# Kernel optimization log

Hardware: AMD Instinct MI355X
Metric: run time of the kernel (lower is better)

Reference implementation:

```python
import jax, jax.numpy as jnp
import numpy as np

H = 1024   # hidden_size
S = 1024   # seq_length
B = 32     # batch_size


def setup_inputs() -> dict:
    key = jax.random.key(0)
    k1, k2, k3, k4, k5, k6 = jax.random.split(key, 6)
    scale = 1.0 / np.sqrt(3 * H)
    return {
        "encoder_states": jax.random.normal(k1, (S, B, 2 * H), dtype=jnp.float32),
        "hidden": jax.random.normal(k2, (B, H), dtype=jnp.float32),
        "cell": jax.random.normal(k3, (B, H), dtype=jnp.float32),
        "W_attn": jax.random.normal(k4, (H, 3 * H), dtype=jnp.float32) * scale,
        "b_attn": jax.random.normal(k5, (H,), dtype=jnp.float32) * scale,
        "v_w": jax.random.normal(k6, (H,), dtype=jnp.float32) * (1.0 / np.sqrt(H)),
    }


def reference(encoder_states, hidden, cell, W_attn, b_attn, v_w):
    # cell is accepted by the original forward but unused.
    # Split the concat-linear into two projections (mathematically identical,
    # avoids materializing the repeated hidden + concat tensor):
    # cat((hidden_rep, enc), -1) @ W.T == hidden @ W[:, :H].T + enc @ W[:, H:].T
    W_h = W_attn[:, :H]          # [H, H]   multiplies decoder hidden
    W_e = W_attn[:, H:]          # [H, 2H]  multiplies encoder states
    enc = jnp.transpose(encoder_states, (1, 0, 2))          # [B, S, 2H]
    h_proj = hidden @ W_h.T + b_attn                         # [B, H], broadcast over S
    e_proj = jnp.einsum("bse,he->bsh", enc, W_e)             # [B, S, H]
    energy = jnp.tanh(h_proj[:, None, :] + e_proj)           # [B, S, H]
    attention = jnp.einsum("bsh,h->bs", energy, v_w)         # [B, S]
    return jax.nn.softmax(attention, axis=1)
```

## Files before the change

kernel.cpp:

```cpp
#include <hip/hip_runtime.h>
#include <hip/hip_bf16.h>

#define H 1024
#define S 1024
#define B 32
#define K2 2048

typedef unsigned short u16;
typedef __attribute__((ext_vector_type(8))) short short8;
typedef __attribute__((ext_vector_type(8))) unsigned short u16x8;
typedef __attribute__((ext_vector_type(4))) float floatx4;

__device__ __forceinline__ u16 f2bf(float f) {
  unsigned u = __float_as_uint(f);
  u += 0x7FFFu + ((u >> 16) & 1u);
  return (u16)(u >> 16);
}

__device__ __forceinline__ void gld_lds16(const void* g, void* l) {
  __builtin_amdgcn_global_load_lds(
      (const __attribute__((address_space(1))) unsigned int*)g,
      (__attribute__((address_space(3))) unsigned int*)l, 16, 0, 0);
}

__global__ void conv_we_k(const float* __restrict__ W, u16* __restrict__ dst) {
  const int h = blockIdx.x;
  const int t = threadIdx.x * 8;
  const float* sp = W + (size_t)h * 3072 + H + t;
  u16* dp = dst + (size_t)h * K2 + t;
  floatx4 x = *(const floatx4*)sp;
  floatx4 y = *(const floatx4*)(sp + 4);
  u16x8 o;
  o[0] = f2bf(x[0]); o[1] = f2bf(x[1]); o[2] = f2bf(x[2]); o[3] = f2bf(x[3]);
  o[4] = f2bf(y[0]); o[5] = f2bf(y[1]); o[6] = f2bf(y[2]); o[7] = f2bf(y[3]);
  *(u16x8*)dp = o;
}

__global__ void conv_enc_k(const float* __restrict__ enc, u16* __restrict__ dst) {
  const int sb = blockIdx.x;
  const int s = sb >> 5;
  const int b = sb & 31;
  const int t = threadIdx.x * 8;
  const float* sp = enc + (size_t)sb * K2 + t;
  u16* dp = dst + ((size_t)b * S + s) * K2 + t;
  floatx4 x = *(const floatx4*)sp;
  floatx4 y = *(const floatx4*)(sp + 4);
  u16x8 o;
  o[0] = f2bf(x[0]); o[1] = f2bf(x[1]); o[2] = f2bf(x[2]); o[3] = f2bf(x[3]);
  o[4] = f2bf(y[0]); o[5] = f2bf(y[1]); o[6] = f2bf(y[2]); o[7] = f2bf(y[3]);
  *(u16x8*)dp = o;
}

__global__ void hproj_k(const float* __restrict__ hidden, const float* __restrict__ W,
                        const float* __restrict__ b_attn, float* __restrict__ hp) {
  const int lane = threadIdx.x & 63;
  const int h = (blockIdx.x * blockDim.x + threadIdx.x) >> 6;
  float wr[16];
#pragma unroll
  for (int i = 0; i < 16; i++) wr[i] = W[(size_t)h * 3072 + lane + i * 64];
  for (int b = 0; b < B; b++) {
    float d = 0.f;
#pragma unroll
    for (int i = 0; i < 16; i++) d = fmaf(wr[i], hidden[b * H + lane + i * 64], d);
#pragma unroll
    for (int off = 32; off; off >>= 1) d += __shfl_xor(d, off);
    if (lane == 0) hp[b * H + h] = d + b_attn[h];
  }
}

#define BM 128
#define BN 128
#define BK 32

__global__ __launch_bounds__(256) void gemm_bf16_2ph_k(
    const u16* __restrict__ A,
    const u16* __restrict__ Bw,
    const float* __restrict__ hp, const float* __restrict__ vw,
    float* __restrict__ attn) {
  __shared__ __align__(16) u16 sA[2][BM * BK];
  __shared__ __align__(16) u16 sB[2][BN * BK];
  const int tid = threadIdx.x;
  const int bid = blockIdx.x;
  const int ntile = bid & 7;
  const int mtile = (bid >> 3) & 7;
  const int b = bid >> 6;
  const int s0 = mtile * BM;
  const int h0 = ntile * BN;

  const int lane = tid & 63;
  const int wv = tid >> 6;
  const int wm = (wv >> 1) * 64;
  const int wn = (wv & 1) * 64;
  const int fr = lane & 15;
  const int kgrp = lane >> 4;

  const int lr4 = lane >> 2, sg4 = lane & 3;

  const u16* Abase = A + (size_t)b * S * K2;

  floatx4 acc[4][4];
#pragma unroll
  for (int i = 0; i < 4; i++)
#pragma unroll
    for (int j = 0; j < 4; j++) acc[i][j] = (floatx4){0.f, 0.f, 0.f, 0.f};

#pragma unroll
  for (int p = 0; p < 2; p++) {
    const int r = wv * 32 + p * 16 + lr4;
    gld_lds16(Abase + (size_t)(s0 + r) * K2 + ((sg4 ^ ((r >> 1) & 3)) << 3),
              (char*)sA[0] + (wv * 32 + p * 16) * 64);
    gld_lds16(Bw + (size_t)(h0 + r) * K2 + ((sg4 ^ ((r >> 1) & 3)) << 3),
              (char*)sB[0] + (wv * 32 + p * 16) * 64);
  }
  __syncthreads();

  for (int t = 0; t < K2 / BK; ++t) {
    const int c = t & 1;
    const int k1 = (t + 1) * BK;
    if (k1 < K2) {
#pragma unroll
      for (int p = 0; p < 2; p++) {
        const int r = wv * 32 + p * 16 + lr4;
        gld_lds16(Abase + (size_t)(s0 + r) * K2 + k1 + ((sg4 ^ ((r >> 1) & 3)) << 3),
                  (char*)sA[1 - c] + (wv * 32 + p * 16) * 64);
        gld_lds16(Bw + (size_t)(h0 + r) * K2 + k1 + ((sg4 ^ ((r >> 1) & 3)) << 3),
                  (char*)sB[1 - c] + (wv * 32 + p * 16) * 64);
      }
    }
    short8 af[4], bfr[4];
#pragma unroll
    for (int mf = 0; mf < 4; mf++) {
      const int R = wm + mf * 16 + fr;
      af[mf] = *(const short8*)&sA[c][R * BK + ((kgrp ^ ((R >> 1) & 3)) << 3)];
    }
#pragma unroll
    for (int nf = 0; nf < 4; nf++) {
      const int R = wn + nf * 16 + fr;
      bfr[nf] = *(const short8*)&sB[c][R * BK + ((kgrp ^ ((R >> 1) & 3)) << 3)];
    }
#pragma unroll
    for (int mf = 0; mf < 4; mf++)
#pragma unroll
      for (int nf = 0; nf < 4; nf++)
        acc[mf][nf] =
            __builtin_amdgcn_mfma_f32_16x16x32_bf16(af[mf], bfr[nf], acc[mf][nf], 0, 0, 0);
    __syncthreads();
  }

  const int col = fr;
  const int rgrp = lane >> 4;
  float hv[4], vv[4];
#pragma unroll
  for (int nf = 0; nf < 4; nf++) {
    const int h = h0 + wn + nf * 16 + col;
    hv[nf] = hp[b * H + h];
    vv[nf] = vw[h];
  }
#pragma unroll
  for (int mf = 0; mf < 4; mf++) {
#pragma unroll
    for (int r = 0; r < 4; r++) {
      float part = 0.f;
#pragma unroll
      for (int nf = 0; nf < 4; nf++) part += tanhf(acc[mf][nf][r] + hv[nf]) * vv[nf];
      part += __shfl_xor(part, 1);
      part += __shfl_xor(part, 2);
      part += __shfl_xor(part, 4);
      part += __shfl_xor(part, 8);
      if (col == 0)
        atomicAdd(&attn[b * S + s0 + wm + mf * 16 + rgrp * 4 + r], part);
    }
  }
}

__global__ void softmax_k(const float* __restrict__ attn, float* __restrict__ out) {
  __shared__ float red[8];
  const int b = blockIdx.x;
  const int tid = threadIdx.x;
  const float* row = attn + b * S;
  float v[4];
#pragma unroll
  for (int i = 0; i < 4; i++) v[i] = row[tid + i * 256];
  float m = fmaxf(fmaxf(v[0], v[1]), fmaxf(v[2], v[3]));
#pragma unroll
  for (int off = 32; off; off >>= 1) m = fmaxf(m, __shfl_xor(m, off));
  if ((tid & 63) == 0) red[tid >> 6] = m;
  __syncthreads();
  m = fmaxf(fmaxf(red[0], red[1]), fmaxf(red[2], red[3]));
  float e[4], sum = 0.f;
#pragma unroll
  for (int i = 0; i < 4; i++) { e[i] = __expf(v[i] - m); sum += e[i]; }
#pragma unroll
  for (int off = 32; off; off >>= 1) sum += __shfl_xor(sum, off);
  __syncthreads();
  if ((tid & 63) == 0) red[4 + (tid >> 6)] = sum;
  __syncthreads();
  sum = red[4] + red[5] + red[6] + red[7];
  const float inv = 1.0f / sum;
#pragma unroll
  for (int i = 0; i < 4; i++) out[b * S + tid + i * 256] = e[i] * inv;
}

extern "C" void kernel_launch(void* const* d_in, const int* in_sizes, int n_in,
                              void* d_out, int out_size, void* d_ws, size_t ws_size,
                              hipStream_t stream) {
  const float* enc    = (const float*)d_in[0];
  const float* hidden = (const float*)d_in[1];
  const float* W_attn = (const float*)d_in[3];
  const float* b_attn = (const float*)d_in[4];
  const float* v_w    = (const float*)d_in[5];
  float* out = (float*)d_out;

  char* ws = (char*)d_ws;
  float* attn = (float*)ws;
  float* hp   = (float*)(ws + 131072);
  u16* Web    = (u16*)(ws + 262144);
  u16* encb   = (u16*)(ws + 4456448);

  hipMemsetAsync(attn, 0, B * S * sizeof(float), stream);
  conv_we_k<<<H, 256, 0, stream>>>(W_attn, Web);
  hproj_k<<<256, 256, 0, stream>>>(hidden, W_attn, b_attn, hp);
  conv_enc_k<<<S * B, 256, 0, stream>>>(enc, encb);
  gemm_bf16_2ph_k<<<2048, 256, 0, stream>>>(encb, Web, hp, v_w, attn);
  softmax_k<<<B, 256, 0, stream>>>(attn, out);
}
```

Measured before the change: 631.4 us.

## Use single-buffered BK=64 GEMM tiles, reorder block mapping, and fast tanh

The GEMM K-tile doubles from 32 to 64 with an 8-way XOR swizzle, and the double-buffered LDS prefetch becomes single buffering with two syncs per iteration. Blocks are remapped so consecutive blocks share the same weight N-tile across batches and M-tiles, which should improve L2 reuse of the weights. The epilogue swaps tanhf for an exp-based fast tanh. Dropping the prefetch loses the overlap of global loads with MFMA work. The fast tanh can lose accuracy or overflow to inf for large inputs, though 1-2/(inf+1) still evaluates to 1.

Result: no change. 638.2 us (+1.1%).

```diff
diff --git a/kernel.cpp b/kernel.cpp
--- a/kernel.cpp
+++ b/kernel.cpp
@@ -21,6 +21,11 @@
   __builtin_amdgcn_global_load_lds(
       (const __attribute__((address_space(1))) unsigned int*)g,
       (__attribute__((address_space(3))) unsigned int*)l, 16, 0, 0);
+}
+
+__device__ __forceinline__ float tanh_fast(float x) {
+  float t = __expf(2.0f * x);
+  return 1.0f - 2.0f / (t + 1.0f);
 }
 
 __global__ void conv_we_k(const float* __restrict__ W, u16* __restrict__ dst) {
@@ -70,20 +75,20 @@
 
 #define BM 128
 #define BN 128
-#define BK 32
-
-__global__ __launch_bounds__(256) void gemm_bf16_2ph_k(
+#define BK 64
+
+__global__ __launch_bounds__(256) void gemm_bf16_k(
     const u16* __restrict__ A,
     const u16* __restrict__ Bw,
     const float* __restrict__ hp, const float* __restrict__ vw,
     float* __restrict__ attn) {
-  __shared__ __align__(16) u16 sA[2][BM * BK];
-  __shared__ __align__(16) u16 sB[2][BN * BK];
+  __shared__ __align__(16) u16 sA[BM * BK];
+  __shared__ __align__(16) u16 sB[BN * BK];
   const int tid = threadIdx.x;
   const int bid = blockIdx.x;
-  const int ntile = bid & 7;
-  const int mtile = (bid >> 3) & 7;
-  const int b = bid >> 6;
+  const int ntile = bid >> 8;
+  const int b = (bid & 255) >> 3;
+  const int mtile = bid & 7;
   const int s0 = mtile * BM;
   const int h0 = ntile * BN;
 
@@ -94,7 +99,9 @@
   const int fr = lane & 15;
   const int kgrp = lane >> 4;
 
-  const int lr4 = lane >> 2, sg4 = lane & 3;
+  const int lr8 = lane >> 3;
+  const int sg8 = lane & 7;
+  const int ssw = (sg8 ^ lr8) << 3;
 
   const u16* Abase = A + (size_t)b * S * K2;
 
@@ -104,47 +111,39 @@
 #pragma unroll
     for (int j = 0; j < 4; j++) acc[i][j] = (floatx4){0.f, 0.f, 0.f, 0.f};
 
-#pragma unroll
-  for (int p = 0; p < 2; p++) {
-    const int r = wv * 32 + p * 16 + lr4;
-    gld_lds16(Abase + (size_t)(s0 + r) * K2 + ((sg4 ^ ((r >> 1) & 3)) << 3),
-              (char*)sA[0] + (wv * 32 + p * 16) * 64);
-    gld_lds16(Bw + (size_t)(h0 + r) * K2 + ((sg4 ^ ((r >> 1) & 3)) << 3),
-              (char*)sB[0] + (wv * 32 + p * 16) * 64);
-  }
-  __syncthreads();
-
-  for (int t = 0; t < K2 / BK; ++t) {
-    const int c = t & 1;
-    const int k1 = (t + 1) * BK;
-    if (k1 < K2) {
-#pragma unroll
-      for (int p = 0; p < 2; p++) {
-        const int r = wv * 32 + p * 16 + lr4;
-        gld_lds16(Abase + (size_t)(s0 + r) * K2 + k1 + ((sg4 ^ ((r >> 1) & 3)) << 3),
-                  (char*)sA[1 - c] + (wv * 32 + p * 16) * 64);
-        gld_lds16(Bw + (size_t)(h0 + r) * K2 + k1 + ((sg4 ^ ((r >> 1) & 3)) << 3),
-                  (char*)sB[1 - c] + (wv * 32 + p * 16) * 64);
+  for (int k0 = 0; k0 < K2; k0 += BK) {
+    __syncthreads();
+#pragma unroll
+    for (int p = 0; p < 4; p++) {
+      const int r = p * 32 + wv * 8 + lr8;
+      gld_lds16(Abase + (size_t)(s0 + r) * K2 + k0 + ssw,
+                (char*)sA + (p * 32 + wv * 8) * 128);
+      gld_lds16(Bw + (size_t)(h0 + r) * K2 + k0 + ssw,
+                (char*)sB + (p * 32 + wv * 8) * 128);
+    }
+    __syncthreads();
+
+#pragma unroll
+    for (int kh = 0; kh < 2; ++kh) {
+      const int ks = kh * 4 + kgrp;
+      short8 af[4], bfr[4];
+#pragma unroll
+      for (int mf = 0; mf < 4; mf++) {
+        const int R = wm + mf * 16 + fr;
+        af[mf] = *(const short8*)&sA[R * BK + ((ks ^ (R & 7)) << 3)];
       }
+#pragma unroll
+      for (int nf = 0; nf < 4; nf++) {
+        const int R = wn + nf * 16 + fr;
+        bfr[nf] = *(const short8*)&sB[R * BK + ((ks ^ (R & 7)) << 3)];
+      }
+#pragma unroll
+      for (int mf = 0; mf < 4; mf++)
+#pragma unroll
+        for (int nf = 0; nf < 4; nf++)
+          acc[mf][nf] =
+              __builtin_amdgcn_mfma_f32_16x16x32_bf16(af[mf], bfr[nf], acc[mf][nf], 0, 0, 0);
     }
-    short8 af[4], bfr[4];
-#pragma unroll
-    for (int mf = 0; mf < 4; mf++) {
-      const int R = wm + mf * 16 + fr;
-      af[mf] = *(const short8*)&sA[c][R * BK + ((kgrp ^ ((R >> 1) & 3)) << 3)];
-    }
-#pragma unroll
-    for (int nf = 0; nf < 4; nf++) {
-      const int R = wn + nf * 16 + fr;
-      bfr[nf] = *(const short8*)&sB[c][R * BK + ((kgrp ^ ((R >> 1) & 3)) << 3)];
-    }
-#pragma unroll
-    for (int mf = 0; mf < 4; mf++)
-#pragma unroll
-      for (int nf = 0; nf < 4; nf++)
-        acc[mf][nf] =
-            __builtin_amdgcn_mfma_f32_16x16x32_bf16(af[mf], bfr[nf], acc[mf][nf], 0, 0, 0);
-    __syncthreads();
   }
 
   const int col = fr;
@@ -162,7 +161,7 @@
     for (int r = 0; r < 4; r++) {
       float part = 0.f;
 #pragma unroll
-      for (int nf = 0; nf < 4; nf++) part += tanhf(acc[mf][nf][r] + hv[nf]) * vv[nf];
+      for (int nf = 0; nf < 4; nf++) part += tanh_fast(acc[mf][nf][r] + hv[nf]) * vv[nf];
       part += __shfl_xor(part, 1);
       part += __shfl_xor(part, 2);
       part += __shfl_xor(part, 4);
@@ -221,6 +220,6 @@
   conv_we_k<<<H, 256, 0, stream>>>(W_attn, Web);
   hproj_k<<<256, 256, 0, stream>>>(hidden, W_attn, b_attn, hp);
   conv_enc_k<<<S * B, 256, 0, stream>>>(enc, encb);
-  gemm_bf16_2ph_k<<<2048, 256, 0, stream>>>(encb, Web, hp, v_w, attn);
+  gemm_bf16_k<<<2048, 256, 0, stream>>>(encb, Web, hp, v_w, attn);
   softmax_k<<<B, 256, 0, stream>>>(attn, out);
 }
```
